# Kernel tuning notes

Measured on AMD Instinct MI355X. Metric: run time of the kernel, lower is better.

## Reference

```python
import jax, jax.numpy as jnp
import numpy as np

B, C_IN, C_OUT, NLAT, NLON = 64, 8, 8, 128, 256
M0, M1 = 16, 16
IN_FLAT = 2 * C_IN * M0 * M1      # 4096
HID = 4 * C_OUT * M0 * M1         # 8192
MMAX_I = NLON // 2 + 1            # 129 frequencies kept by rfft / used by isht


def _cc_nodes_weights(n):
    """Clenshaw-Curtis nodes cos(pi*j/(n-1)) and quadrature weights on [-1,1]."""
    N = n - 1
    tj = np.pi * np.arange(n) / N
    xlg = np.cos(tj)
    w = np.full(n, 2.0 / N)
    for k in range(1, N // 2 + 1):
        bk = 1.0 if 2 * k == N else 2.0
        w -= bk * np.cos(2.0 * k * tj) * (2.0 / N) / (4.0 * k * k - 1.0)
    w[0] *= 0.5
    w[-1] *= 0.5
    return xlg, w


def _legpoly(mmax, lmax, x):
    """Ortho-normalized associated Legendre P_l^m(x) with Condon-Shortley phase.
    Returns (mmax, lmax, len(x)); mirrors torch_harmonics legpoly recurrence."""
    nmax = max(mmax, lmax)
    vdm = np.zeros((nmax, nmax, len(x)))
    vdm[0, 0] = 1.0 / np.sqrt(4.0 * np.pi)
    for l in range(1, nmax):
        vdm[l - 1, l] = np.sqrt(2.0 * l + 1.0) * x * vdm[l - 1, l - 1]
        vdm[l, l] = np.sqrt((2.0 * l + 1.0) * (1.0 + x) * (1.0 - x) / 2.0 / l) * vdm[l - 1, l - 1]
    for l in range(2, nmax):
        for m in range(l - 1):
            a = np.sqrt((2.0 * l - 1.0) / (l - m) * (2.0 * l + 1.0) / (l + m))
            b = np.sqrt((l + m - 1.0) / (l - m) * (2.0 * l + 1.0) / (2.0 * l - 3.0) * (l - m - 1.0) / (l + m))
            vdm[m, l] = a * x * vdm[m, l - 1] - b * vdm[m, l - 2]
    vdm = vdm[:mmax, :lmax]
    vdm[1::2] *= -1.0  # Condon-Shortley phase on odd m
    return vdm


_xlg, _wq = _cc_nodes_weights(NLAT)
_ct = _xlg[::-1].copy()  # cos(flip(arccos(xlg))), as in torch_harmonics
# forward SHT weights: legpoly * quadrature weights, shape (M1, M0, NLAT)
W_FWD = jnp.asarray(_legpoly(M1, M0, _ct) * _wq[None, None, :], dtype=jnp.float32)
# inverse SHT basis, shape (MMAX_I, NLAT, NLAT) = (m, l, lat)
PCT_INV = jnp.asarray(_legpoly(MMAX_I, NLAT, _ct), dtype=jnp.float32)


def _sfno_forward(x, w0, b0, w1, conv_w, conv_b):
    Bsz = x.shape[0]
    # --- forward real SHT, truncated to (M0, M1) modes (norm='ortho', forward-normalized FFT) ---
    xf = (2.0 * jnp.pi / NLON) * jnp.fft.rfft(x, axis=-1)        # (B,C,NLAT,NLON//2+1) complex
    xf = xf[..., :M1]                                             # keep M1 longitudinal modes
    xh = jnp.einsum('bckm,mlk->bclm', xf, W_FWD)                  # (B,C,M0,M1) complex
    # --- mode-truncated complex MLP: flatten (real,imag) pairs, Linear-GELU-Linear ---
    z = jnp.stack((xh.real, xh.imag), axis=-1).reshape(Bsz, -1)   # (B, 2*C*M0*M1)
    z = jax.nn.gelu(z @ w0.T + b0, approximate=False)
    z = z @ w1.T
    z = z.reshape(Bsz, C_OUT, M0, M1, 2)
    oh = jax.lax.complex(z[..., 0], z[..., 1])                    # (B,C_out,M0,M1) complex
    # --- scatter back into zero-padded full coefficient tensor ---
    full = jnp.zeros((Bsz, C_OUT, NLAT, MMAX_I), dtype=jnp.complex64)
    full = full.at[:, :, :M0, :M1].set(oh)
    # --- inverse real SHT (norm='ortho', irfft with norm='forward' => unscaled inverse) ---
    xk = jnp.einsum('bclm,mlk->bckm', full, PCT_INV)              # (B,C_out,NLAT,MMAX_I)
    spec = jnp.fft.irfft(xk, n=NLON, axis=-1) * NLON              # (B,C_out,NLAT,NLON)
    # --- 1x1 bypass conv + activation ---
    bypass = jnp.einsum('bchw,oc->bohw', x, conv_w) + conv_b[None, :, None, None]
    return jax.nn.gelu(spec + bypass, approximate=False)


def setup_inputs() -> dict:
    key = jax.random.key(0)
    ks = jax.random.split(key, 6)
    x = jax.random.normal(ks[0], (B, C_IN, NLAT, NLON), dtype=jnp.float32)
    w0 = jax.random.normal(ks[1], (HID, IN_FLAT), dtype=jnp.float32) / np.sqrt(IN_FLAT)
    b0 = jax.random.normal(ks[2], (HID,), dtype=jnp.float32) * 0.01
    w1 = jax.random.normal(ks[3], (2 * C_OUT * M0 * M1, HID), dtype=jnp.float32) / np.sqrt(HID)
    conv_w = jax.random.normal(ks[4], (C_OUT, C_IN), dtype=jnp.float32) / np.sqrt(C_IN)
    conv_b = jax.random.normal(ks[5], (C_OUT,), dtype=jnp.float32) * 0.01
    return {"x": x, "w0": w0, "b0": b0, "w1": w1, "conv_w": conv_w, "conv_b": conv_b}


def reference(x, w0, b0, w1, conv_w, conv_b):
    return _sfno_forward(x, w0, b0, w1, conv_w, conv_b)
```

## Files before the change

### kernel.cpp

```cpp
#include <hip/hip_runtime.h>
#include <hip/hip_bf16.h>
#include <math.h>

typedef float  f32x4 __attribute__((ext_vector_type(4)));
typedef _Float16 f16x8 __attribute__((ext_vector_type(8)));
typedef short  s16x8 __attribute__((ext_vector_type(8)));

#define WFWDT_OFF  0u
#define PCTT_OFF   131072u
#define FFRAG_OFF  262144u
#define TBFRAG_OFF 278528u
#define Z_OFF      294912u
#define H_OFF      819200u
#define OH_OFF     1867776u

static __device__ __forceinline__ float gelu_f(float v) {
  return 0.5f * v * (1.0f + erff(v * 0.70710678118654752f));
}
static __device__ __forceinline__ unsigned short f2bf(float a) {
  union { __hip_bfloat16 h; unsigned short u; } cv;
  cv.h = __float2bfloat16(a);
  return cv.u;
}
static __device__ __forceinline__ unsigned int pack_bf2(float a, float b) {
  return (unsigned int)f2bf(a) | ((unsigned int)f2bf(b) << 16);
}

__global__ __launch_bounds__(256) void k0_tables(float* __restrict__ wfwdt,
    float* __restrict__ pctt, _Float16* __restrict__ ffrag, _Float16* __restrict__ tbfrag) {
  const int tid = threadIdx.x;
  const double PI = 3.14159265358979323846;
  if (tid < 128) {
    const int k = tid;
    const double xx = cos(PI * (double)(127 - k) / 127.0);
    const double tj = PI * (double)k / 127.0;
    double wq = 2.0 / 127.0;
    for (int qq = 1; qq <= 63; ++qq)
      wq -= 2.0 * cos(2.0 * qq * tj) * (2.0 / 127.0) / (4.0 * (double)qq * qq - 1.0);
    if (k == 0 || k == 127) wq *= 0.5;

    double prev2[16], prev1[16], cur[16];
    double diag = 0.28209479177387814347;
    for (int m = 0; m < 16; ++m) { prev2[m] = 0.0; prev1[m] = 0.0; cur[m] = 0.0; }
    cur[0] = diag;
    for (int m = 0; m < 16; ++m) {
      double v = cur[m] * ((m & 1) ? -1.0 : 1.0);
      wfwdt[k*256 + m] = (float)(v * wq);
      pctt [k*256 + m] = (float)v;
      prev1[m] = cur[m];
    }
    for (int l = 1; l < 16; ++l) {
      double nd  = sqrt((2.0*l + 1.0) * (1.0 + xx) * (1.0 - xx) / (2.0 * l)) * diag;
      double sup = sqrt(2.0*l + 1.0) * xx * diag;
      for (int m = 0; m < 16; ++m) cur[m] = 0.0;
      for (int m = 0; m <= l - 2; ++m) {
        double a  = sqrt((2.0*l - 1.0)/(double)(l - m) * (2.0*l + 1.0)/(double)(l + m));
        double bb = sqrt(((double)l + m - 1.0)/(double)(l - m) * (2.0*l + 1.0)/(2.0*l - 3.0)
                         * ((double)l - m - 1.0)/(double)(l + m));
        cur[m] = a * xx * prev1[m] - bb * prev2[m];
      }
      cur[l-1] = sup;
      cur[l]   = nd;
      for (int m = 0; m < 16; ++m) {
        double v = cur[m] * ((m & 1) ? -1.0 : 1.0);
        wfwdt[k*256 + l*16 + m] = (float)(v * wq);
        pctt [k*256 + l*16 + m] = (float)v;
        prev2[m] = prev1[m]; prev1[m] = cur[m];
      }
      diag = nd;
    }
  }
  const double S = 2.0 * PI / 256.0;
  for (int i = tid; i < 8192; i += 256) {
    const int j = i & 7, ln = (i >> 3) & 63, blk = i >> 9;
    {
      const int nt = blk & 1, kc = blk >> 1;
      const int w = kc*32 + (ln >> 4)*8 + j;
      const int kap = nt*16 + (ln & 15);
      const int m = kap >> 1;
      const double th = S * (double)((m * w) & 255);
      const double v = (kap & 1) ? (-S * sin(th)) : (S * cos(th));
      ffrag[i] = (_Float16)(float)v;
    }
    {
      const int wt = blk;
      const int w = wt*16 + (ln & 15);
      const int kap = (ln >> 4)*8 + j;
      const int m = kap >> 1;
      const double th = S * (double)((m * w) & 255);
      double v;
      if (kap & 1) v = (m == 0) ? 0.0 : (-2.0 * sin(th));
      else         v = (m == 0) ? 1.0 : ( 2.0 * cos(th));
      tbfrag[i] = (_Float16)(float)v;
    }
  }
}

__global__ __launch_bounds__(256) void k1_fwd(const float* __restrict__ x,
    const float* __restrict__ wfwdt, const _Float16* __restrict__ ffrag,
    unsigned short* __restrict__ z) {
  __shared__ _Float16 sF[8192];
  __shared__ float sxf[128 * 34];
  const int tid = threadIdx.x;
  const int lane = tid & 63, wv = tid >> 6;
  const int n = lane & 15, q = lane >> 4;
  const int bc = blockIdx.x;
  {
    const uint4* src = (const uint4*)ffrag;
    uint4* dst = (uint4*)sF;
    for (int i = tid; i < 1024; i += 256) dst[i] = src[i];
  }
  __syncthreads();
  f32x4 acc[2][2];
  for (int a1 = 0; a1 < 2; ++a1) for (int a2 = 0; a2 < 2; ++a2)
    acc[a1][a2] = (f32x4){0.f, 0.f, 0.f, 0.f};
  const float* xb = x + (size_t)bc * 32768;
  for (int kc = 0; kc < 8; ++kc) {
    f16x8 bfr0 = *(const f16x8*)&sF[((kc*2 + 0)*64 + lane)*8];
    f16x8 bfr1 = *(const f16x8*)&sF[((kc*2 + 1)*64 + lane)*8];
#pragma unroll
    for (int rtl = 0; rtl < 2; ++rtl) {
      const int row = (2*wv + rtl)*16 + n;
      const float* p = xb + row*256 + kc*32 + q*8;
      f32x4 v0 = *(const f32x4*)p;
      f32x4 v1 = *(const f32x4*)(p + 4);
      f16x8 afr;
      afr[0] = (_Float16)v0.x; afr[1] = (_Float16)v0.y;
      afr[2] = (_Float16)v0.z; afr[3] = (_Float16)v0.w;
      afr[4] = (_Float16)v1.x; afr[5] = (_Float16)v1.y;
      afr[6] = (_Float16)v1.z; afr[7] = (_Float16)v1.w;
      acc[rtl][0] = __builtin_amdgcn_mfma_f32_16x16x32_f16(afr, bfr0, acc[rtl][0], 0, 0, 0);
      acc[rtl][1] = __builtin_amdgcn_mfma_f32_16x16x32_f16(afr, bfr1, acc[rtl][1], 0, 0, 0);
    }
  }
#pragma unroll
  for (int rtl = 0; rtl < 2; ++rtl)
#pragma unroll
    for (int nt = 0; nt < 2; ++nt)
#pragma unroll
      for (int r = 0; r < 4; ++r)
        sxf[((2*wv + rtl)*16 + q*4 + r)*34 + nt*16 + n] = acc[rtl][nt][r];
  __syncthreads();
  const int m = tid & 15, l = tid >> 4;
  float zre = 0.f, zim = 0.f;
  const float* wp = wfwdt + l*16 + m;
#pragma unroll 4
  for (int k = 0; k < 128; ++k) {
    const float wk = wp[k*256];
    zre += wk * sxf[k*34 + 2*m];
    zim += wk * sxf[k*34 + 2*m + 1];
  }
  const int b = bc >> 3, c = bc & 7;
  *(unsigned int*)&z[(size_t)b*4096 + c*512 + l*32 + 2*m] = pack_bf2(zre, zim);
}

__global__ __launch_bounds__(256) void k2_mlp1(const unsigned short* __restrict__ z,
    const float* __restrict__ w0, const float* __restrict__ bias0,
    unsigned short* __restrict__ h) {
  __shared__ short sB[8192];
  const int tid = threadIdx.x, lane = tid & 63, wv = tid >> 6;
  const int n = lane & 15, q = lane >> 4;
  const int h0 = blockIdx.x * 32;
  int se[4]; size_t sgl[4];
#pragma unroll
  for (int i = 0; i < 4; ++i) {
    const int e = i*256 + tid;
    const int blk = e >> 6, ls = e & 63;
    const int s = blk >> 1, nt = blk & 1;
    se[i] = e;
    sgl[i] = (size_t)(h0 + nt*16 + (ls & 15))*4096 + s*32 + (ls >> 4)*8;
  }
  f32x4 pfa[4], pfb[4];
#pragma unroll
  for (int i = 0; i < 4; ++i) {
    const float* p = &w0[sgl[i]];
    pfa[i] = *(const f32x4*)p; pfb[i] = *(const f32x4*)(p + 4);
  }
  f32x4 acc0 = {0.f,0.f,0.f,0.f}, acc1 = {0.f,0.f,0.f,0.f};
  const unsigned short* zp = z + (size_t)(wv*16 + n)*4096 + q*8;
  for (int kc = 0; kc < 16; ++kc) {
    __syncthreads();
#pragma unroll
    for (int i = 0; i < 4; ++i) {
      union { unsigned int u[4]; uint4 v; } pk;
      pk.u[0] = pack_bf2(pfa[i].x, pfa[i].y);
      pk.u[1] = pack_bf2(pfa[i].z, pfa[i].w);
      pk.u[2] = pack_bf2(pfb[i].x, pfb[i].y);
      pk.u[3] = pack_bf2(pfb[i].z, pfb[i].w);
      *(uint4*)&sB[se[i]*8] = pk.v;
    }
    __syncthreads();
    if (kc < 15) {
#pragma unroll
      for (int i = 0; i < 4; ++i) {
        const float* p = &w0[sgl[i] + (size_t)(kc + 1)*256];
        pfa[i] = *(const f32x4*)p; pfb[i] = *(const f32x4*)(p + 4);
      }
    }
#pragma unroll
    for (int s = 0; s < 8; ++s) {
      s16x8 afr = *(const s16x8*)(zp + (size_t)kc*256 + s*32);
      s16x8 bf0 = *(const s16x8*)&sB[((s*2 + 0)*64 + lane)*8];
      s16x8 bf1 = *(const s16x8*)&sB[((s*2 + 1)*64 + lane)*8];
      acc0 = __builtin_amdgcn_mfma_f32_16x16x32_bf16(afr, bf0, acc0, 0, 0, 0);
      acc1 = __builtin_amdgcn_mfma_f32_16x16x32_bf16(afr, bf1, acc1, 0, 0, 0);
    }
  }
#pragma unroll
  for (int nt = 0; nt < 2; ++nt) {
    f32x4 a = nt ? acc1 : acc0;
    const int col = h0 + nt*16 + n;
    const float bias = bias0[col];
#pragma unroll
    for (int r = 0; r < 4; ++r) {
      const int row = wv*16 + q*4 + r;
      h[(size_t)row*8192 + col] = f2bf(gelu_f(a[r] + bias));
    }
  }
}

__global__ __launch_bounds__(256) void k3_mlp2(const unsigned short* __restrict__ h,
    const float* __restrict__ w1, float* __restrict__ oh) {
  __shared__ short sB[4096];
  const int tid = threadIdx.x, lane = tid & 63, wv = tid >> 6;
  const int n = lane & 15, q = lane >> 4;
  const int j0 = blockIdx.x * 16;
  int se[2]; size_t sgl[2];
#pragma unroll
  for (int i = 0; i < 2; ++i) {
    const int e = i*256 + tid;
    const int s = e >> 6, ls = e & 63;
    se[i] = e;
    sgl[i] = (size_t)(j0 + (ls & 15))*8192 + s*32 + (ls >> 4)*8;
  }
  f32x4 pfa[2], pfb[2];
#pragma unroll
  for (int i = 0; i < 2; ++i) {
    const float* p = &w1[sgl[i]];
    pfa[i] = *(const f32x4*)p; pfb[i] = *(const f32x4*)(p + 4);
  }
  f32x4 acc = {0.f,0.f,0.f,0.f};
  const unsigned short* hp = h + (size_t)(wv*16 + n)*8192 + q*8;
  for (int kc = 0; kc < 32; ++kc) {
    __syncthreads();
#pragma unroll
    for (int i = 0; i < 2; ++i) {
      union { unsigned int u[4]; uint4 v; } pk;
      pk.u[0] = pack_bf2(pfa[i].x, pfa[i].y);
      pk.u[1] = pack_bf2(pfa[i].z, pfa[i].w);
      pk.u[2] = pack_bf2(pfb[i].x, pfb[i].y);
      pk.u[3] = pack_bf2(pfb[i].z, pfb[i].w);
      *(uint4*)&sB[se[i]*8] = pk.v;
    }
    __syncthreads();
    if (kc < 31) {
#pragma unroll
      for (int i = 0; i < 2; ++i) {
        const float* p = &w1[sgl[i] + (size_t)(kc + 1)*256];
        pfa[i] = *(const f32x4*)p; pfb[i] = *(const f32x4*)(p + 4);
      }
    }
#pragma unroll
    for (int s = 0; s < 8; ++s) {
      s16x8 afr = *(const s16x8*)(hp + (size_t)kc*256 + s*32);
      s16x8 bfr = *(const s16x8*)&sB[(s*64 + lane)*8];
      acc = __builtin_amdgcn_mfma_f32_16x16x32_bf16(afr, bfr, acc, 0, 0, 0);
    }
  }
#pragma unroll
  for (int r = 0; r < 4; ++r)
    oh[(size_t)(wv*16 + q*4 + r)*4096 + j0 + n] = acc[r];
}

__global__ __launch_bounds__(256) void k4_inv(const float* __restrict__ oh,
    const float* __restrict__ pctt, const _Float16* __restrict__ tbfrag,
    const float* __restrict__ x, const float* __restrict__ cw,
    const float* __restrict__ cb, float* __restrict__ out) {
  __shared__ float soh[4096];
  __shared__ float spct[4096];
  __shared__ _Float16 sTB[8192];
  __shared__ _Float16 sXK[128 * 40];
  __shared__ float scw[64];
  __shared__ float scb[8];
  const int tid = threadIdx.x, lane = tid & 63, wv = tid >> 6;
  const int n = lane & 15, q = lane >> 4;
  const int b = blockIdx.x >> 3, k0 = (blockIdx.x & 7) * 16;
  {
    const f32x4* s1 = (const f32x4*)(oh + (size_t)b*4096);
    const f32x4* s2 = (const f32x4*)(pctt + (size_t)k0*256);
    const uint4* s3 = (const uint4*)tbfrag;
    for (int i = tid; i < 1024; i += 256) {
      ((f32x4*)soh)[i]  = s1[i];
      ((f32x4*)spct)[i] = s2[i];
      ((uint4*)sTB)[i]  = s3[i];
    }
    if (tid < 64) scw[tid] = cw[tid];
    if (tid < 8)  scb[tid] = cb[tid];
  }
  __syncthreads();
#pragma unroll
  for (int i = 0; i < 8; ++i) {
    const int p = i*256 + tid;
    const int row = p >> 4, m = p & 15;
    const int cc = row >> 4, kk = row & 15;
    float re = 0.f, im = 0.f;
    const float* op = soh + cc*512 + m*2;
    const float* pp = spct + kk*256 + m;
#pragma unroll
    for (int l = 0; l < 16; ++l) {
      const float pv = pp[l*16];
      re += pv * op[l*32];
      im += pv * op[l*32 + 1];
    }
    sXK[row*40 + 2*m]     = (_Float16)re;
    sXK[row*40 + 2*m + 1] = (_Float16)im;
  }
  __syncthreads();
  const f16x8 afr0 = *(const f16x8*)&sXK[((2*wv + 0)*16 + n)*40 + q*8];
  const f16x8 afr1 = *(const f16x8*)&sXK[((2*wv + 1)*16 + n)*40 + q*8];
  float cw0[8], cw1[8];
#pragma unroll
  for (int ci = 0; ci < 8; ++ci) {
    cw0[ci] = scw[(2*wv + 0)*8 + ci];
    cw1[ci] = scw[(2*wv + 1)*8 + ci];
  }
  const float cb0 = scb[2*wv], cb1 = scb[2*wv + 1];
  for (int wt = 0; wt < 16; ++wt) {
    const f16x8 bfr = *(const f16x8*)&sTB[(wt*64 + lane)*8];
    f32x4 z4 = {0.f,0.f,0.f,0.f};
    f32x4 a0 = __builtin_amdgcn_mfma_f32_16x16x32_f16(afr0, bfr, z4, 0, 0, 0);
    f32x4 a1 = __builtin_amdgcn_mfma_f32_16x16x32_f16(afr1, bfr, z4, 0, 0, 0);
    const int w = wt*16 + n;
    float bp0[4] = {0.f,0.f,0.f,0.f}, bp1[4] = {0.f,0.f,0.f,0.f};
    const float* xp = x + ((size_t)b*1024 + (size_t)(k0 + q*4))*256 + w;
#pragma unroll
    for (int ci = 0; ci < 8; ++ci) {
      const float* xq = xp + (size_t)ci*32768;
      const float c0 = cw0[ci], c1 = cw1[ci];
#pragma unroll
      for (int r = 0; r < 4; ++r) {
        const float xv = xq[r*256];
        bp0[r] += xv * c0;
        bp1[r] += xv * c1;
      }
    }
    float* op0 = out + (((size_t)b*8 + 2*wv + 0)*128 + k0 + q*4)*256 + w;
    float* op1 = out + (((size_t)b*8 + 2*wv + 1)*128 + k0 + q*4)*256 + w;
#pragma unroll
    for (int r = 0; r < 4; ++r) {
      op0[r*256] = gelu_f(a0[r] + bp0[r] + cb0);
      op1[r*256] = gelu_f(a1[r] + bp1[r] + cb1);
    }
  }
}

extern "C" void kernel_launch(void* const* d_in, const int* in_sizes, int n_in,
                              void* d_out, int out_size, void* d_ws, size_t ws_size,
                              hipStream_t stream) {
  (void)in_sizes; (void)n_in; (void)out_size; (void)ws_size;
  const float* x   = (const float*)d_in[0];
  const float* w0  = (const float*)d_in[1];
  const float* b0v = (const float*)d_in[2];
  const float* w1  = (const float*)d_in[3];
  const float* cw  = (const float*)d_in[4];
  const float* cb  = (const float*)d_in[5];
  float* out = (float*)d_out;
  char* ws = (char*)d_ws;
  float* wfwdt        = (float*)(ws + WFWDT_OFF);
  float* pctt         = (float*)(ws + PCTT_OFF);
  _Float16* ffrag     = (_Float16*)(ws + FFRAG_OFF);
  _Float16* tbfr      = (_Float16*)(ws + TBFRAG_OFF);
  unsigned short* z   = (unsigned short*)(ws + Z_OFF);
  unsigned short* h   = (unsigned short*)(ws + H_OFF);
  float* oh           = (float*)(ws + OH_OFF);

  hipLaunchKernelGGL(k0_tables, dim3(1),   dim3(256), 0, stream, wfwdt, pctt, ffrag, tbfr);
  hipLaunchKernelGGL(k1_fwd,    dim3(512), dim3(256), 0, stream, x, wfwdt, ffrag, z);
  hipLaunchKernelGGL(k2_mlp1,   dim3(256), dim3(256), 0, stream, z, w0, b0v, h);
  hipLaunchKernelGGL(k3_mlp2,   dim3(256), dim3(256), 0, stream, h, w1, oh);
  hipLaunchKernelGGL(k4_inv,    dim3(512), dim3(256), 0, stream, oh, pctt, tbfr, x, cw, cb, out);
}
```

Baseline: 514.2 us.

## Split MLP GEMMs across more blocks, deepen weight prefetch, parallelize table setup

The first MLP GEMM now uses 16-column tiles, so it launches 512 blocks instead of 256. The second GEMM splits K in half across 512 blocks, writes two partial outputs, and the inverse kernel sums them when it loads. Both GEMMs now prefetch weights two K-steps ahead with double-buffered registers. Table setup is split across two blocks, with LDS trig lookups, a Chebyshev recurrence for the quadrature weights, and precomputed recurrence coefficients. The goal is better CU occupancy for the bandwidth-bound weight streaming and a shorter serial setup kernel. The cost is extra partial-sum traffic and more registers per thread.

Result: faster. 435.4 us (-15.3%).

```diff
diff --git a/kernel.cpp b/kernel.cpp
--- a/kernel.cpp
+++ b/kernel.cpp
@@ -13,6 +13,7 @@
 #define Z_OFF      294912u
 #define H_OFF      819200u
 #define OH_OFF     1867776u
+#define OH1_OFF    2916352u
 
 static __device__ __forceinline__ float gelu_f(float v) {
   return 0.5f * v * (1.0f + erff(v * 0.70710678118654752f));
@@ -30,69 +31,93 @@
     float* __restrict__ pctt, _Float16* __restrict__ ffrag, _Float16* __restrict__ tbfrag) {
   const int tid = threadIdx.x;
   const double PI = 3.14159265358979323846;
-  if (tid < 128) {
-    const int k = tid;
-    const double xx = cos(PI * (double)(127 - k) / 127.0);
-    const double tj = PI * (double)k / 127.0;
-    double wq = 2.0 / 127.0;
-    for (int qq = 1; qq <= 63; ++qq)
-      wq -= 2.0 * cos(2.0 * qq * tj) * (2.0 / 127.0) / (4.0 * (double)qq * qq - 1.0);
+  if (blockIdx.x == 1) {
+    __shared__ float lc[256], ls2[256];
+    {
+      const double th = 2.0 * PI * (double)tid / 256.0;
+      lc[tid]  = (float)cos(th);
+      ls2[tid] = (float)sin(th);
+    }
+    __syncthreads();
+    const float S = (float)(2.0 * PI / 256.0);
+    for (int i = tid; i < 8192; i += 256) {
+      const int j = i & 7, ln = (i >> 3) & 63, blk = i >> 9;
+      {
+        const int nt = blk & 1, kc = blk >> 1;
+        const int w = kc*32 + (ln >> 4)*8 + j;
+        const int kap = nt*16 + (ln & 15);
+        const int m = kap >> 1;
+        const int a = (m * w) & 255;
+        const float v = (kap & 1) ? (-S * ls2[a]) : (S * lc[a]);
+        ffrag[i] = (_Float16)v;
+      }
+      {
+        const int wt = blk;
+        const int w = wt*16 + (ln & 15);
+        const int kap = (ln >> 4)*8 + j;
+        const int m = kap >> 1;
+        const int a = (m * w) & 255;
+        float v;
+        if (kap & 1) v = (m == 0) ? 0.0f : (-2.0f * ls2[a]);
+        else         v = (m == 0) ? 1.0f : ( 2.0f * lc[a]);
+        tbfrag[i] = (_Float16)v;
+      }
+    }
+    return;
+  }
+  __shared__ double cA[256], cB[256];
+  {
+    const int l = tid >> 4, m = tid & 15;
+    double a = 0.0, bb = 0.0;
+    if (l >= 2 && m <= l - 2) {
+      a  = sqrt((2.0*l - 1.0)/(double)(l - m) * (2.0*l + 1.0)/(double)(l + m));
+      bb = sqrt(((double)l + m - 1.0)/(double)(l - m) * (2.0*l + 1.0)/(2.0*l - 3.0)
+                * ((double)l - m - 1.0)/(double)(l + m));
+    }
+    cA[tid] = a; cB[tid] = bb;
+  }
+  __syncthreads();
+  if (tid >= 128) return;
+  const int k = tid;
+  const double xx = cos(PI * (double)(127 - k) / 127.0);
+  const double tj = PI * (double)k / 127.0;
+  double wq = 2.0 / 127.0;
+  {
+    const double t2 = cos(2.0 * tj);
+    double cm1 = 1.0, c = t2;
+    for (int qq = 1; qq <= 63; ++qq) {
+      wq -= 2.0 * c * (2.0 / 127.0) / (4.0 * (double)qq * qq - 1.0);
+      const double cn = 2.0 * t2 * c - cm1;
+      cm1 = c; c = cn;
+    }
     if (k == 0 || k == 127) wq *= 0.5;
-
-    double prev2[16], prev1[16], cur[16];
-    double diag = 0.28209479177387814347;
-    for (int m = 0; m < 16; ++m) { prev2[m] = 0.0; prev1[m] = 0.0; cur[m] = 0.0; }
-    cur[0] = diag;
+  }
+  double prev2[16], prev1[16], cur[16];
+  double diag = 0.28209479177387814347;
+  for (int m = 0; m < 16; ++m) { prev2[m] = 0.0; prev1[m] = 0.0; }
+  cur[0] = diag;
+  for (int m = 1; m < 16; ++m) cur[m] = 0.0;
+  for (int m = 0; m < 16; ++m) {
+    double v = cur[m] * ((m & 1) ? -1.0 : 1.0);
+    wfwdt[k*256 + m] = (float)(v * wq);
+    pctt [k*256 + m] = (float)v;
+    prev1[m] = cur[m];
+  }
+  for (int l = 1; l < 16; ++l) {
+    const double nd  = sqrt((2.0*l + 1.0) * (1.0 + xx) * (1.0 - xx) / (2.0 * l)) * diag;
+    const double sup = sqrt(2.0*l + 1.0) * xx * diag;
+    for (int m = 0; m < 16; ++m) cur[m] = 0.0;
+    for (int m = 0; m <= l - 2; ++m)
+      cur[m] = cA[l*16 + m] * xx * prev1[m] - cB[l*16 + m] * prev2[m];
+    cur[l-1] = sup;
+    cur[l]   = nd;
     for (int m = 0; m < 16; ++m) {
       double v = cur[m] * ((m & 1) ? -1.0 : 1.0);
-      wfwdt[k*256 + m] = (float)(v * wq);
-      pctt [k*256 + m] = (float)v;
-      prev1[m] = cur[m];
-    }
-    for (int l = 1; l < 16; ++l) {
-      double nd  = sqrt((2.0*l + 1.0) * (1.0 + xx) * (1.0 - xx) / (2.0 * l)) * diag;
-      double sup = sqrt(2.0*l + 1.0) * xx * diag;
-      for (int m = 0; m < 16; ++m) cur[m] = 0.0;
-      for (int m = 0; m <= l - 2; ++m) {
-        double a  = sqrt((2.0*l - 1.0)/(double)(l - m) * (2.0*l + 1.0)/(double)(l + m));
-        double bb = sqrt(((double)l + m - 1.0)/(double)(l - m) * (2.0*l + 1.0)/(2.0*l - 3.0)
-                         * ((double)l - m - 1.0)/(double)(l + m));
-        cur[m] = a * xx * prev1[m] - bb * prev2[m];
-      }
-      cur[l-1] = sup;
-      cur[l]   = nd;
-      for (int m = 0; m < 16; ++m) {
-        double v = cur[m] * ((m & 1) ? -1.0 : 1.0);
-        wfwdt[k*256 + l*16 + m] = (float)(v * wq);
-        pctt [k*256 + l*16 + m] = (float)v;
-        prev2[m] = prev1[m]; prev1[m] = cur[m];
-      }
-      diag = nd;
-    }
-  }
-  const double S = 2.0 * PI / 256.0;
-  for (int i = tid; i < 8192; i += 256) {
-    const int j = i & 7, ln = (i >> 3) & 63, blk = i >> 9;
-    {
-      const int nt = blk & 1, kc = blk >> 1;
-      const int w = kc*32 + (ln >> 4)*8 + j;
-      const int kap = nt*16 + (ln & 15);
-      const int m = kap >> 1;
-      const double th = S * (double)((m * w) & 255);
-      const double v = (kap & 1) ? (-S * sin(th)) : (S * cos(th));
-      ffrag[i] = (_Float16)(float)v;
-    }
-    {
-      const int wt = blk;
-      const int w = wt*16 + (ln & 15);
-      const int kap = (ln >> 4)*8 + j;
-      const int m = kap >> 1;
-      const double th = S * (double)((m * w) & 255);
-      double v;
-      if (kap & 1) v = (m == 0) ? 0.0 : (-2.0 * sin(th));
-      else         v = (m == 0) ? 1.0 : ( 2.0 * cos(th));
-      tbfrag[i] = (_Float16)(float)v;
-    }
+      wfwdt[k*256 + l*16 + m] = (float)(v * wq);
+      pctt [k*256 + l*16 + m] = (float)v;
+      prev2[m] = prev1[m]; prev1[m] = cur[m];
+    }
+    diag = nd;
   }
 }
 
@@ -157,107 +182,108 @@
 __global__ __launch_bounds__(256) void k2_mlp1(const unsigned short* __restrict__ z,
     const float* __restrict__ w0, const float* __restrict__ bias0,
     unsigned short* __restrict__ h) {
-  __shared__ short sB[8192];
-  const int tid = threadIdx.x, lane = tid & 63, wv = tid >> 6;
-  const int n = lane & 15, q = lane >> 4;
-  const int h0 = blockIdx.x * 32;
-  int se[4]; size_t sgl[4];
-#pragma unroll
-  for (int i = 0; i < 4; ++i) {
-    const int e = i*256 + tid;
-    const int blk = e >> 6, ls = e & 63;
-    const int s = blk >> 1, nt = blk & 1;
-    se[i] = e;
-    sgl[i] = (size_t)(h0 + nt*16 + (ls & 15))*4096 + s*32 + (ls >> 4)*8;
-  }
-  f32x4 pfa[4], pfb[4];
-#pragma unroll
-  for (int i = 0; i < 4; ++i) {
-    const float* p = &w0[sgl[i]];
-    pfa[i] = *(const f32x4*)p; pfb[i] = *(const f32x4*)(p + 4);
-  }
-  f32x4 acc0 = {0.f,0.f,0.f,0.f}, acc1 = {0.f,0.f,0.f,0.f};
-  const unsigned short* zp = z + (size_t)(wv*16 + n)*4096 + q*8;
-  for (int kc = 0; kc < 16; ++kc) {
-    __syncthreads();
-#pragma unroll
-    for (int i = 0; i < 4; ++i) {
-      union { unsigned int u[4]; uint4 v; } pk;
-      pk.u[0] = pack_bf2(pfa[i].x, pfa[i].y);
-      pk.u[1] = pack_bf2(pfa[i].z, pfa[i].w);
-      pk.u[2] = pack_bf2(pfb[i].x, pfb[i].y);
-      pk.u[3] = pack_bf2(pfb[i].z, pfb[i].w);
-      *(uint4*)&sB[se[i]*8] = pk.v;
-    }
-    __syncthreads();
-    if (kc < 15) {
-#pragma unroll
-      for (int i = 0; i < 4; ++i) {
-        const float* p = &w0[sgl[i] + (size_t)(kc + 1)*256];
-        pfa[i] = *(const f32x4*)p; pfb[i] = *(const f32x4*)(p + 4);
-      }
-    }
-#pragma unroll
-    for (int s = 0; s < 8; ++s) {
-      s16x8 afr = *(const s16x8*)(zp + (size_t)kc*256 + s*32);
-      s16x8 bf0 = *(const s16x8*)&sB[((s*2 + 0)*64 + lane)*8];
-      s16x8 bf1 = *(const s16x8*)&sB[((s*2 + 1)*64 + lane)*8];
-      acc0 = __builtin_amdgcn_mfma_f32_16x16x32_bf16(afr, bf0, acc0, 0, 0, 0);
-      acc1 = __builtin_amdgcn_mfma_f32_16x16x32_bf16(afr, bf1, acc1, 0, 0, 0);
-    }
-  }
-#pragma unroll
-  for (int nt = 0; nt < 2; ++nt) {
-    f32x4 a = nt ? acc1 : acc0;
-    const int col = h0 + nt*16 + n;
-    const float bias = bias0[col];
-#pragma unroll
-    for (int r = 0; r < 4; ++r) {
-      const int row = wv*16 + q*4 + r;
-      h[(size_t)row*8192 + col] = f2bf(gelu_f(a[r] + bias));
-    }
-  }
-}
-
-__global__ __launch_bounds__(256) void k3_mlp2(const unsigned short* __restrict__ h,
-    const float* __restrict__ w1, float* __restrict__ oh) {
   __shared__ short sB[4096];
   const int tid = threadIdx.x, lane = tid & 63, wv = tid >> 6;
   const int n = lane & 15, q = lane >> 4;
-  const int j0 = blockIdx.x * 16;
+  const int h0 = blockIdx.x * 16;
   int se[2]; size_t sgl[2];
 #pragma unroll
   for (int i = 0; i < 2; ++i) {
     const int e = i*256 + tid;
     const int s = e >> 6, ls = e & 63;
     se[i] = e;
-    sgl[i] = (size_t)(j0 + (ls & 15))*8192 + s*32 + (ls >> 4)*8;
-  }
-  f32x4 pfa[2], pfb[2];
-#pragma unroll
-  for (int i = 0; i < 2; ++i) {
-    const float* p = &w1[sgl[i]];
-    pfa[i] = *(const f32x4*)p; pfb[i] = *(const f32x4*)(p + 4);
-  }
+    sgl[i] = (size_t)(h0 + (ls & 15))*4096 + s*32 + (ls >> 4)*8;
+  }
+  f32x4 pfa[2][2], pfb[2][2];
+#pragma unroll
+  for (int d = 0; d < 2; ++d)
+#pragma unroll
+    for (int i = 0; i < 2; ++i) {
+      const float* p = &w0[sgl[i] + (size_t)d*256];
+      pfa[d][i] = *(const f32x4*)p; pfb[d][i] = *(const f32x4*)(p + 4);
+    }
   f32x4 acc = {0.f,0.f,0.f,0.f};
-  const unsigned short* hp = h + (size_t)(wv*16 + n)*8192 + q*8;
-  for (int kc = 0; kc < 32; ++kc) {
+  const unsigned short* zp = z + (size_t)(wv*16 + n)*4096 + q*8;
+  for (int kc = 0; kc < 16; ++kc) {
+    const int pp = kc & 1;
     __syncthreads();
 #pragma unroll
     for (int i = 0; i < 2; ++i) {
       union { unsigned int u[4]; uint4 v; } pk;
-      pk.u[0] = pack_bf2(pfa[i].x, pfa[i].y);
-      pk.u[1] = pack_bf2(pfa[i].z, pfa[i].w);
-      pk.u[2] = pack_bf2(pfb[i].x, pfb[i].y);
-      pk.u[3] = pack_bf2(pfb[i].z, pfb[i].w);
+      pk.u[0] = pack_bf2(pfa[pp][i].x, pfa[pp][i].y);
+      pk.u[1] = pack_bf2(pfa[pp][i].z, pfa[pp][i].w);
+      pk.u[2] = pack_bf2(pfb[pp][i].x, pfb[pp][i].y);
+      pk.u[3] = pack_bf2(pfb[pp][i].z, pfb[pp][i].w);
       *(uint4*)&sB[se[i]*8] = pk.v;
     }
     __syncthreads();
-    if (kc < 31) {
+    if (kc < 14) {
 #pragma unroll
       for (int i = 0; i < 2; ++i) {
-        const float* p = &w1[sgl[i] + (size_t)(kc + 1)*256];
-        pfa[i] = *(const f32x4*)p; pfb[i] = *(const f32x4*)(p + 4);
+        const float* p = &w0[sgl[i] + (size_t)(kc + 2)*256];
+        pfa[pp][i] = *(const f32x4*)p; pfb[pp][i] = *(const f32x4*)(p + 4);
+      }
+    }
+#pragma unroll
+    for (int s = 0; s < 8; ++s) {
+      s16x8 afr = *(const s16x8*)(zp + (size_t)kc*256 + s*32);
+      s16x8 bfr = *(const s16x8*)&sB[(s*64 + lane)*8];
+      acc = __builtin_amdgcn_mfma_f32_16x16x32_bf16(afr, bfr, acc, 0, 0, 0);
+    }
+  }
+  const int col = h0 + n;
+  const float bias = bias0[col];
+#pragma unroll
+  for (int r = 0; r < 4; ++r) {
+    const int row = wv*16 + q*4 + r;
+    h[(size_t)row*8192 + col] = f2bf(gelu_f(acc[r] + bias));
+  }
+}
+
+__global__ __launch_bounds__(256) void k3_mlp2(const unsigned short* __restrict__ h,
+    const float* __restrict__ w1, float* __restrict__ oh0, float* __restrict__ oh1) {
+  __shared__ short sB[4096];
+  const int tid = threadIdx.x, lane = tid & 63, wv = tid >> 6;
+  const int n = lane & 15, q = lane >> 4;
+  const int j0 = (blockIdx.x >> 1) * 16;
+  const int kh = blockIdx.x & 1;
+  const size_t kbase = (size_t)kh * 4096;
+  int se[2]; size_t sgl[2];
+#pragma unroll
+  for (int i = 0; i < 2; ++i) {
+    const int e = i*256 + tid;
+    const int s = e >> 6, ls = e & 63;
+    se[i] = e;
+    sgl[i] = (size_t)(j0 + (ls & 15))*8192 + kbase + s*32 + (ls >> 4)*8;
+  }
+  f32x4 pfa[2][2], pfb[2][2];
+#pragma unroll
+  for (int d = 0; d < 2; ++d)
+#pragma unroll
+    for (int i = 0; i < 2; ++i) {
+      const float* p = &w1[sgl[i] + (size_t)d*256];
+      pfa[d][i] = *(const f32x4*)p; pfb[d][i] = *(const f32x4*)(p + 4);
+    }
+  f32x4 acc = {0.f,0.f,0.f,0.f};
+  const unsigned short* hp = h + (size_t)(wv*16 + n)*8192 + kbase + q*8;
+  for (int kc = 0; kc < 16; ++kc) {
+    const int pp = kc & 1;
+    __syncthreads();
+#pragma unroll
+    for (int i = 0; i < 2; ++i) {
+      union { unsigned int u[4]; uint4 v; } pk;
+      pk.u[0] = pack_bf2(pfa[pp][i].x, pfa[pp][i].y);
+      pk.u[1] = pack_bf2(pfa[pp][i].z, pfa[pp][i].w);
+      pk.u[2] = pack_bf2(pfb[pp][i].x, pfb[pp][i].y);
+      pk.u[3] = pack_bf2(pfb[pp][i].z, pfb[pp][i].w);
+      *(uint4*)&sB[se[i]*8] = pk.v;
+    }
+    __syncthreads();
+    if (kc < 14) {
+#pragma unroll
+      for (int i = 0; i < 2; ++i) {
+        const float* p = &w1[sgl[i] + (size_t)(kc + 2)*256];
+        pfa[pp][i] = *(const f32x4*)p; pfb[pp][i] = *(const f32x4*)(p + 4);
       }
     }
 #pragma unroll
@@ -267,12 +293,14 @@
       acc = __builtin_amdgcn_mfma_f32_16x16x32_bf16(afr, bfr, acc, 0, 0, 0);
     }
   }
+  float* ohp = kh ? oh1 : oh0;
 #pragma unroll
   for (int r = 0; r < 4; ++r)
-    oh[(size_t)(wv*16 + q*4 + r)*4096 + j0 + n] = acc[r];
-}
-
-__global__ __launch_bounds__(256) void k4_inv(const float* __restrict__ oh,
+    ohp[(size_t)(wv*16 + q*4 + r)*4096 + j0 + n] = acc[r];
+}
+
+__global__ __launch_bounds__(256) void k4_inv(const float* __restrict__ oh0,
+    const float* __restrict__ oh1,
     const float* __restrict__ pctt, const _Float16* __restrict__ tbfrag,
     const float* __restrict__ x, const float* __restrict__ cw,
     const float* __restrict__ cb, float* __restrict__ out) {
@@ -286,11 +314,13 @@
   const int n = lane & 15, q = lane >> 4;
   const int b = blockIdx.x >> 3, k0 = (blockIdx.x & 7) * 16;
   {
-    const f32x4* s1 = (const f32x4*)(oh + (size_t)b*4096);
+    const f32x4* s1a = (const f32x4*)(oh0 + (size_t)b*4096);
+    const f32x4* s1b = (const f32x4*)(oh1 + (size_t)b*4096);
     const f32x4* s2 = (const f32x4*)(pctt + (size_t)k0*256);
     const uint4* s3 = (const uint4*)tbfrag;
     for (int i = tid; i < 1024; i += 256) {
-      ((f32x4*)soh)[i]  = s1[i];
+      f32x4 va = s1a[i], vb = s1b[i];
+      ((f32x4*)soh)[i]  = va + vb;
       ((f32x4*)spct)[i] = s2[i];
       ((uint4*)sTB)[i]  = s3[i];
     }
@@ -372,11 +402,12 @@
   _Float16* tbfr      = (_Float16*)(ws + TBFRAG_OFF);
   unsigned short* z   = (unsigned short*)(ws + Z_OFF);
   unsigned short* h   = (unsigned short*)(ws + H_OFF);
-  float* oh           = (float*)(ws + OH_OFF);
-
-  hipLaunchKernelGGL(k0_tables, dim3(1),   dim3(256), 0, stream, wfwdt, pctt, ffrag, tbfr);
+  float* oh0          = (float*)(ws + OH_OFF);
+  float* oh1          = (float*)(ws + OH1_OFF);
+
+  hipLaunchKernelGGL(k0_tables, dim3(2),   dim3(256), 0, stream, wfwdt, pctt, ffrag, tbfr);
   hipLaunchKernelGGL(k1_fwd,    dim3(512), dim3(256), 0, stream, x, wfwdt, ffrag, z);
-  hipLaunchKernelGGL(k2_mlp1,   dim3(256), dim3(256), 0, stream, z, w0, b0v, h);
-  hipLaunchKernelGGL(k3_mlp2,   dim3(256), dim3(256), 0, stream, h, w1, oh);
-  hipLaunchKernelGGL(k4_inv,    dim3(512), dim3(256), 0, stream, oh, pctt, tbfr, x, cw, cb, out);
-}
+  hipLaunchKernelGGL(k2_mlp1,   dim3(512), dim3(256), 0, stream, z, w0, b0v, h);
+  hipLaunchKernelGGL(k3_mlp2,   dim3(512), dim3(256), 0, stream, h, w1, oh0, oh1);
+  hipLaunchKernelGGL(k4_inv,    dim3(512), dim3(256), 0, stream, oh0, oh1, pctt, tbfr, x, cw, cb, out);
+}
```
